# Performance work log

Measured on AMD Instinct MI355X. Metric: run time of the kernel, lower is better.

## Reference

```python
import jax, jax.numpy as jnp
import numpy as np

# BTT dims for in=out=4096, square mode: m=n=64, a=b=64, rank=8
M, N, A, B_BLK, RANK = 64, 64, 64, 64, 8
OUT_FEATURES = M * A  # 4096


def setup_inputs() -> dict:
    key = jax.random.key(0)
    k_x, k_r, k_l = jax.random.split(key, 3)
    x = jax.random.normal(k_x, (4, 1024, 4096), dtype=jnp.float32)
    # btt_r: (n, b, m*rank); btt_l: (m, rank*n, a)
    btt_r = jax.random.normal(k_r, (N, B_BLK, M * RANK), dtype=jnp.float32) * 0.02
    btt_l = jax.random.normal(k_l, (M, RANK * N, A), dtype=jnp.float32) * 0.02
    bias = jnp.zeros((OUT_FEATURES,), dtype=jnp.float32)
    return {"x": x, "btt_r": btt_r, "btt_l": btt_l, "bias": bias}


def reference(x, btt_r, btt_l, bias):
    n, b, mr = btt_r.shape
    m, rn, a = btt_l.shape
    rank = mr // m
    orig_shape = x.shape
    xr = x.reshape(-1, n, b)          # (B, n, b)
    Bn = xr.shape[0]
    # first contraction: bmm over n blocks -> (n, B, m*rank)
    inner = jnp.einsum('Bnb,nbj->nBj', xr, btt_r)
    # reshape/permute exactly as torch: (n,B,m,r) -> (m,B,n,r) -> (m,B,n*r)
    inner = inner.reshape(n, Bn, m, rank).transpose(2, 1, 0, 3).reshape(m, Bn, rank * n)
    # second contraction: bmm over m blocks -> (B, m, a)
    out = jnp.einsum('mBk,mka->Bma', inner, btt_l)
    out = out.reshape(*orig_shape[:-1], m * a)
    return out + bias
```

## Files before the change

kernel.cpp:

```cpp
#include <hip/hip_runtime.h>


typedef float f32x16 __attribute__((ext_vector_type(16)));
typedef short short8 __attribute__((ext_vector_type(8)));

static __device__ __forceinline__ unsigned short f2b(float f) {
    union { float f; unsigned u; } a; a.f = f;
    unsigned u = a.u;
    unsigned r = u + 0x7fffu + ((u >> 16) & 1u);
    return (unsigned short)(r >> 16);
}

static __device__ __forceinline__ void load_lds_16(const void* gptr, void* lptr) {
    __builtin_amdgcn_global_load_lds(
        (const __attribute__((address_space(1))) unsigned int*)gptr,
        (__attribute__((address_space(3))) unsigned int*)lptr, 16, 0, 0);
}

__global__ __launch_bounds__(256) void prep_all(
    const float* __restrict__ x,
    const float* __restrict__ btt_r,
    const float* __restrict__ btt_l,
    unsigned short* __restrict__ xbt,
    unsigned short* __restrict__ Wtt,
    int nx)
{
    const int tid = threadIdx.x;
    if ((int)blockIdx.x < nx) {
        unsigned i = blockIdx.x * 256 + tid;
        int row = ((i >> 12) << 3) | (i & 7);
        int g   = (i >> 3) & 511;
        float4 v0 = *(const float4*)(x + (size_t)row * 4096 + g * 8);
        float4 v1 = *(const float4*)(x + (size_t)row * 4096 + g * 8 + 4);
        unsigned short o[8];
        o[0] = f2b(v0.x); o[1] = f2b(v0.y); o[2] = f2b(v0.z); o[3] = f2b(v0.w);
        o[4] = f2b(v1.x); o[5] = f2b(v1.y); o[6] = f2b(v1.z); o[7] = f2b(v1.w);
        int ks = g >> 1, half = g & 1;
        int rt = row >> 8, rb = (row >> 5) & 7, l31 = row & 31;
        size_t dst = ((((size_t)rt * 256 + ks) * 8 + rb) * 64 + half * 32 + l31) * 8;
        *(uint4*)(xbt + dst) = *(const uint4*)o;
        return;
    }
    __shared__ float Rs[64][8];
    __shared__ float Ls[8][64];
    const int wb = blockIdx.x - nx;
    const int m = wb >> 6, n = wb & 63;

    if (tid < 128) {
        int b = tid >> 1, rh = (tid & 1) * 4;
        float4 v = *(const float4*)(btt_r + (size_t)n * 32768 + (size_t)b * 512 + m * 8 + rh);
        *(float4*)&Rs[b][rh] = v;
    } else {
        int t2 = (tid - 128) * 4;
        float4 v = *(const float4*)(btt_l + (size_t)m * 32768 + n * 512 + t2);
        *(float4*)&(&Ls[0][0])[t2] = v;
    }
    __syncthreads();

    const int a  = tid >> 2;
    const int bg = (tid & 3) * 16;
    float la[8];
    #pragma unroll
    for (int r = 0; r < 8; ++r) la[r] = Ls[r][a];

    unsigned short o[16];
    #pragma unroll
    for (int bb = 0; bb < 16; ++bb) {
        float acc = 0.f;
        #pragma unroll
        for (int r = 0; r < 8; ++r) acc += Rs[bg + bb][r] * la[r];
        o[bb] = f2b(acc);
    }
    int col = m * 64 + a;
    int ct = col >> 8, rb = (col >> 5) & 7, l31 = col & 31;
    int ks = n * 4 + (bg >> 4);
    size_t dst = ((((size_t)ct * 256 + ks) * 8 + rb) * 64 + l31) * 8;
    *(uint4*)(Wtt + dst)           = *(const uint4*)&o[0];
    *(uint4*)(Wtt + dst + 32 * 8)  = *(const uint4*)&o[8];
}

__global__ __launch_bounds__(512, 2) void gemm_btt(
    const unsigned short* __restrict__ xbt,
    const unsigned short* __restrict__ Wtt,
    const float* __restrict__ bias,
    float* __restrict__ out)
{
    __shared__ unsigned short As[8][4096];
    __shared__ unsigned short Bs[8][4096];

    const int tid = threadIdx.x;
    const int bid = blockIdx.x;
    const int jj = bid >> 3, xc = bid & 7;
    const int rt = (xc >> 1) * 4 + (jj >> 3);
    const int ct = (xc & 1) * 8 + (jj & 7);

    const int wid = tid >> 6, l = tid & 63;
    const int l31 = l & 31, half = l >> 5;
    const int wr = wid >> 2;
    const int wc = wid & 3;

    const unsigned short* xa = xbt + (size_t)rt * (256 * 4096);
    const unsigned short* wa = Wtt + (size_t)ct * (256 * 4096);

    const int offA0 = ((wr * 4 + 0) * 64 + l) * 8;
    const int offA1 = ((wr * 4 + 1) * 64 + l) * 8;
    const int offA2 = ((wr * 4 + 2) * 64 + l) * 8;
    const int offA3 = ((wr * 4 + 3) * 64 + l) * 8;
    const int offB0 = ((wc * 2 + 0) * 64 + l) * 8;
    const int offB1 = ((wc * 2 + 1) * 64 + l) * 8;

    f32x16 acc[4][2];
    #pragma unroll
    for (int i = 0; i < 4; ++i)
        #pragma unroll
        for (int j = 0; j < 2; ++j)
            #pragma unroll
            for (int r = 0; r < 16; ++r)
                acc[i][j][r] = 0.f;

    short8 fA0, fA1, fA2, fA3, fB0, fB1;
    short8 gA0, gA1, gA2, gA3, gB0, gB1;

    #define STAGE(s, slot) do {                                               \
        load_lds_16(xa + (size_t)(s) * 4096 + tid * 8, &As[slot][tid * 8]);   \
        load_lds_16(wa + (size_t)(s) * 4096 + tid * 8, &Bs[slot][tid * 8]);   \
    } while (0)

    #define STAGE2(sa, sla, sb, slb) do {                                     \
        STAGE(sa, sla);                                                       \
        STAGE(sb, slb);                                                       \
    } while (0)

    #define NOSTAGE do { } while (0)

    #define READ6(pA0,pA1,pA2,pA3,pB0,pB1, slot) do {                         \
        const unsigned short* Ab = &As[slot][0];                              \
        const unsigned short* Bb = &Bs[slot][0];                              \
        pA0 = *(const short8*)(Ab + offA0);                                   \
        pA1 = *(const short8*)(Ab + offA1);                                   \
        pA2 = *(const short8*)(Ab + offA2);                                   \
        pA3 = *(const short8*)(Ab + offA3);                                   \
        pB0 = *(const short8*)(Bb + offB0);                                   \
        pB1 = *(const short8*)(Bb + offB1);                                   \
    } while (0)

    #define MFMA8(cA0,cA1,cA2,cA3,cB0,cB1) do {                               \
        acc[0][0] = __builtin_amdgcn_mfma_f32_32x32x16_bf16(cA0, cB0, acc[0][0], 0, 0, 0); \
        acc[0][1] = __builtin_amdgcn_mfma_f32_32x32x16_bf16(cA0, cB1, acc[0][1], 0, 0, 0); \
        acc[1][0] = __builtin_amdgcn_mfma_f32_32x32x16_bf16(cA1, cB0, acc[1][0], 0, 0, 0); \
        acc[1][1] = __builtin_amdgcn_mfma_f32_32x32x16_bf16(cA1, cB1, acc[1][1], 0, 0, 0); \
        acc[2][0] = __builtin_amdgcn_mfma_f32_32x32x16_bf16(cA2, cB0, acc[2][0], 0, 0, 0); \
        acc[2][1] = __builtin_amdgcn_mfma_f32_32x32x16_bf16(cA2, cB1, acc[2][1], 0, 0, 0); \
        acc[3][0] = __builtin_amdgcn_mfma_f32_32x32x16_bf16(cA3, cB0, acc[3][0], 0, 0, 0); \
        acc[3][1] = __builtin_amdgcn_mfma_f32_32x32x16_bf16(cA3, cB1, acc[3][1], 0, 0, 0); \
    } while (0)

    #define SUPER(e, STAGE_STMT, VMSTR) do {                                  \
        asm volatile(VMSTR ::: "memory");                                     \
        __builtin_amdgcn_s_barrier();                                         \
        asm volatile("" ::: "memory");                                        \
        STAGE_STMT;                                                           \
        READ6(fA0,fA1,fA2,fA3,fB0,fB1, (e));                                  \
        READ6(gA0,gA1,gA2,gA3,gB0,gB1, (e) + 1);                              \
        __builtin_amdgcn_s_setprio(1);                                        \
        MFMA8(fA0,fA1,fA2,fA3,fB0,fB1);                                       \
        MFMA8(gA0,gA1,gA2,gA3,gB0,gB1);                                       \
        __builtin_amdgcn_s_setprio(0);                                        \
    } while (0)

    STAGE(0, 0); STAGE(1, 1); STAGE(2, 2); STAGE(3, 3); STAGE(4, 4); STAGE(5, 5);

    #pragma unroll 1
    for (int it2 = 0; it2 < 31; ++it2) {
        const int s8 = it2 * 8;
        SUPER(0, STAGE2(s8 + 6,  6, s8 + 7,  7), "s_waitcnt vmcnt(8)");
        SUPER(2, STAGE2(s8 + 8,  0, s8 + 9,  1), "s_waitcnt vmcnt(8)");
        SUPER(4, STAGE2(s8 + 10, 2, s8 + 11, 3), "s_waitcnt vmcnt(8)");
        SUPER(6, STAGE2(s8 + 12, 4, s8 + 13, 5), "s_waitcnt vmcnt(8)");
    }
    SUPER(0, STAGE2(254, 6, 255, 7), "s_waitcnt vmcnt(8)");
    SUPER(2, NOSTAGE,                "s_waitcnt vmcnt(8)");
    SUPER(4, NOSTAGE,                "s_waitcnt vmcnt(4)");
    SUPER(6, NOSTAGE,                "s_waitcnt vmcnt(0)");

    const int rowTileBase = rt * 256 + wr * 128;
    const int colTileBase = ct * 256 + wc * 64;
    #pragma unroll
    for (int jn = 0; jn < 2; ++jn) {
        const int col = colTileBase + jn * 32 + l31;
        const float bv = bias[col];
        #pragma unroll
        for (int i = 0; i < 4; ++i) {
            const int rbase = rowTileBase + i * 32 + 4 * half;
            #pragma unroll
            for (int r = 0; r < 16; ++r) {
                int row = rbase + (r & 3) + 8 * (r >> 2);
                out[(size_t)row * 4096 + col] = acc[i][jn][r] + bv;
            }
        }
    }
    #undef STAGE
    #undef STAGE2
    #undef NOSTAGE
    #undef READ6
    #undef MFMA8
    #undef SUPER
}

extern "C" void kernel_launch(void* const* d_in, const int* in_sizes, int n_in,
                              void* d_out, int out_size, void* d_ws, size_t ws_size,
                              hipStream_t stream) {
    const float* x    = (const float*)d_in[0];
    const float* r    = (const float*)d_in[1];
    const float* l    = (const float*)d_in[2];
    const float* bias = (const float*)d_in[3];
    float* out = (float*)d_out;

    unsigned short* xbt = (unsigned short*)d_ws;
    unsigned short* Wtt = (unsigned short*)d_ws + (size_t)4096 * 4096;

    const int rows = in_sizes[0] / 4096;
    const int nx = rows * 4096 / 8 / 256;

    prep_all<<<dim3(nx + 4096), dim3(256), 0, stream>>>(x, r, l, xbt, Wtt, nx);
    gemm_btt<<<dim3((rows / 256) * 16), dim3(512), 0, stream>>>(xbt, Wtt, bias, out);
}
```

Before: 278.6 us.

## Split prep into separate x-conversion and weight-build kernels with LDS-staged coalesced stores

Splits the fused preprocessing kernel into two launches: one that converts x to bf16 and one that builds the fused weight. The x path now reads 64 contiguous floats per row through LDS and writes whole contiguous 64-lane tiles, so both global reads and stores are coalesced. The weight path is remapped so each wave writes one contiguous tile chunk and reads R rows with vector LDS loads. This adds one extra kernel launch and an LDS barrier in the x conversion.

```diff
diff --git a/kernel.cpp b/kernel.cpp
--- a/kernel.cpp
+++ b/kernel.cpp
@@ -17,33 +17,56 @@
         (__attribute__((address_space(3))) unsigned int*)lptr, 16, 0, 0);
 }
 
-__global__ __launch_bounds__(256) void prep_all(
-    const float* __restrict__ x,
+__global__ __launch_bounds__(256) void conv_x(
+    const float* __restrict__ x, unsigned short* __restrict__ xbt, int rows)
+{
+    __shared__ unsigned short Lx[8][64][8];
+    const int tid = threadIdx.x;
+    const int bx = blockIdx.x;
+    const int kblk = bx & 63;
+    const int rowblk = bx >> 6;
+
+    const int r6 = tid >> 2, kq = tid & 3;
+    const int row = rowblk * 64 + r6;
+    const float* src = x + (size_t)row * 4096 + kblk * 64 + kq * 16;
+    float4 v0 = *(const float4*)(src + 0);
+    float4 v1 = *(const float4*)(src + 4);
+    float4 v2 = *(const float4*)(src + 8);
+    float4 v3 = *(const float4*)(src + 12);
+    unsigned short o[16];
+    o[0]  = f2b(v0.x); o[1]  = f2b(v0.y); o[2]  = f2b(v0.z); o[3]  = f2b(v0.w);
+    o[4]  = f2b(v1.x); o[5]  = f2b(v1.y); o[6]  = f2b(v1.z); o[7]  = f2b(v1.w);
+    o[8]  = f2b(v2.x); o[9]  = f2b(v2.y); o[10] = f2b(v2.z); o[11] = f2b(v2.w);
+    o[12] = f2b(v3.x); o[13] = f2b(v3.y); o[14] = f2b(v3.z); o[15] = f2b(v3.w);
+    const int rb_l = r6 >> 5, l31 = r6 & 31;
+    const int c = kq * 2 + rb_l;
+    *(uint4*)&Lx[c][0 * 32 + l31][0] = *(const uint4*)&o[0];
+    *(uint4*)&Lx[c][1 * 32 + l31][0] = *(const uint4*)&o[8];
+    __syncthreads();
+
+    const int lane = tid & 63;
+    const int cc0 = tid >> 6;
+    const int rt = rowblk >> 2;
+    #pragma unroll
+    for (int p = 0; p < 2; ++p) {
+        const int cc = cc0 + p * 4;
+        const int ksl = cc >> 1, rbl = cc & 1;
+        const int ks = kblk * 4 + ksl;
+        const int rb = (rowblk & 3) * 2 + rbl;
+        size_t dst = ((((size_t)rt * 256 + ks) * 8 + rb) * 64 + lane) * 8;
+        *(uint4*)(xbt + dst) = *(const uint4*)&Lx[cc][lane][0];
+    }
+}
+
+__global__ __launch_bounds__(256) void prep_w(
     const float* __restrict__ btt_r,
     const float* __restrict__ btt_l,
-    unsigned short* __restrict__ xbt,
-    unsigned short* __restrict__ Wtt,
-    int nx)
+    unsigned short* __restrict__ Wtt)
 {
-    const int tid = threadIdx.x;
-    if ((int)blockIdx.x < nx) {
-        unsigned i = blockIdx.x * 256 + tid;
-        int row = ((i >> 12) << 3) | (i & 7);
-        int g   = (i >> 3) & 511;
-        float4 v0 = *(const float4*)(x + (size_t)row * 4096 + g * 8);
-        float4 v1 = *(const float4*)(x + (size_t)row * 4096 + g * 8 + 4);
-        unsigned short o[8];
-        o[0] = f2b(v0.x); o[1] = f2b(v0.y); o[2] = f2b(v0.z); o[3] = f2b(v0.w);
-        o[4] = f2b(v1.x); o[5] = f2b(v1.y); o[6] = f2b(v1.z); o[7] = f2b(v1.w);
-        int ks = g >> 1, half = g & 1;
-        int rt = row >> 8, rb = (row >> 5) & 7, l31 = row & 31;
-        size_t dst = ((((size_t)rt * 256 + ks) * 8 + rb) * 64 + half * 32 + l31) * 8;
-        *(uint4*)(xbt + dst) = *(const uint4*)o;
-        return;
-    }
     __shared__ float Rs[64][8];
     __shared__ float Ls[8][64];
-    const int wb = blockIdx.x - nx;
+    const int tid = threadIdx.x;
+    const int wb = blockIdx.x;
     const int m = wb >> 6, n = wb & 63;
 
     if (tid < 128) {
@@ -57,26 +80,34 @@
     }
     __syncthreads();
 
-    const int a  = tid >> 2;
-    const int bg = (tid & 3) * 16;
-    float la[8];
-    #pragma unroll
-    for (int r = 0; r < 8; ++r) la[r] = Ls[r][a];
-
-    unsigned short o[16];
-    #pragma unroll
-    for (int bb = 0; bb < 16; ++bb) {
-        float acc = 0.f;
-        #pragma unroll
-        for (int r = 0; r < 8; ++r) acc += Rs[bg + bb][r] * la[r];
-        o[bb] = f2b(acc);
-    }
-    int col = m * 64 + a;
-    int ct = col >> 8, rb = (col >> 5) & 7, l31 = col & 31;
-    int ks = n * 4 + (bg >> 4);
-    size_t dst = ((((size_t)ct * 256 + ks) * 8 + rb) * 64 + l31) * 8;
-    *(uint4*)(Wtt + dst)           = *(const uint4*)&o[0];
-    *(uint4*)(Wtt + dst + 32 * 8)  = *(const uint4*)&o[8];
+    const int lane = tid & 63;
+    const int lc = lane & 31, half = lane >> 5;
+    const int ct = m >> 2;
+    #pragma unroll
+    for (int p = 0; p < 2; ++p) {
+        const int c = p * 4 + (tid >> 6);
+        const int rb = c >> 2, ksl = c & 3;
+        const int col6 = rb * 32 + lc;
+        float la[8];
+        #pragma unroll
+        for (int r = 0; r < 8; ++r) la[r] = Ls[r][col6];
+        const int b0 = ksl * 16 + half * 8;
+        unsigned short o[8];
+        #pragma unroll
+        for (int j = 0; j < 8; ++j) {
+            float4 rv0 = *(const float4*)&Rs[b0 + j][0];
+            float4 rv1 = *(const float4*)&Rs[b0 + j][4];
+            float acc = rv0.x * la[0];
+            acc += rv0.y * la[1]; acc += rv0.z * la[2]; acc += rv0.w * la[3];
+            acc += rv1.x * la[4]; acc += rv1.y * la[5]; acc += rv1.z * la[6];
+            acc += rv1.w * la[7];
+            o[j] = f2b(acc);
+        }
+        const int ks = n * 4 + ksl;
+        const int rbg = (m & 3) * 2 + rb;
+        size_t dst = ((((size_t)ct * 256 + ks) * 8 + rbg) * 64 + lane) * 8;
+        *(uint4*)(Wtt + dst) = *(const uint4*)&o[0];
+    }
 }
 
 __global__ __launch_bounds__(512, 2) void gemm_btt(
@@ -220,8 +251,8 @@
     unsigned short* Wtt = (unsigned short*)d_ws + (size_t)4096 * 4096;
 
     const int rows = in_sizes[0] / 4096;
-    const int nx = rows * 4096 / 8 / 256;
-
-    prep_all<<<dim3(nx + 4096), dim3(256), 0, stream>>>(x, r, l, xbt, Wtt, nx);
+
+    conv_x<<<dim3((rows >> 6) * 64), dim3(256), 0, stream>>>(x, xbt, rows);
+    prep_w<<<dim3(4096), dim3(256), 0, stream>>>(r, l, Wtt);
     gemm_btt<<<dim3((rows / 256) * 16), dim3(512), 0, stream>>>(xbt, Wtt, bias, out);
 }
```

After: 260.9 us. 6.3% less time.
